# Kernel optimization log

Hardware: AMD Instinct MI355X
Metric: run time of the kernel (lower is better)

## Reference

```python
import jax, jax.numpy as jnp
import numpy as np

NUM_CLASSES = 10000
KREG = 5
LAMDA = 0.001
ALLOW_ZERO_SETS = False


def setup_inputs() -> dict:
    key = jax.random.key(0)
    k1, k2 = jax.random.split(key)
    logits = jax.random.normal(k1, (4096, NUM_CLASSES), dtype=jnp.float32)
    u = jax.random.uniform(k2, (4096,), dtype=jnp.float32)  # randomized tie-break draws
    T = jnp.asarray(1.3, dtype=jnp.float32)        # Platt temperature
    Qhat = jnp.asarray(0.9, dtype=jnp.float32)     # calibrated quantile threshold
    penalties = jnp.zeros((1, NUM_CLASSES), dtype=jnp.float32).at[:, KREG:].add(LAMDA)
    return {"logits": logits, "u": u, "T": T, "Qhat": Qhat, "penalties": penalties}


def reference(logits, u, T, Qhat, penalties):
    B, C = logits.shape
    scores = jax.nn.softmax(logits / T, axis=1)                  # [B, C]
    order = jnp.argsort(-scores, axis=1)                          # descending class indices
    ordered = jnp.take_along_axis(scores, order, axis=1)          # sorted scores, desc
    csum = jnp.cumsum(ordered, axis=1)                            # [B, C]
    pcs = jnp.cumsum(penalties, axis=1)                           # [1, C]
    # gcq: base set sizes via cumulative threshold
    sizes_base = jnp.sum((csum + pcs) <= Qhat, axis=1) + 1        # [B]
    sizes_base = jnp.minimum(sizes_base, C)
    # randomized rounding
    rows = jnp.arange(B)
    idx = jnp.maximum(sizes_base - 1, 0)
    ord_i = ordered[rows, idx]
    cs_i = csum[rows, idx]
    pc_i = pcs[0, idx]
    V = (Qhat - (cs_i - ord_i) - pc_i) / ord_i                    # [B]
    sizes = sizes_base - (u >= V).astype(sizes_base.dtype)
    sizes = jnp.where(Qhat == 1.0, C, sizes)
    if not ALLOW_ZERO_SETS:
        sizes = jnp.where(sizes == 0, 1, sizes)
    # Prediction sets S[i] = I[i, :sizes[i]] encoded as a dense membership mask.
    mask_sorted = jnp.arange(C)[None, :] < sizes[:, None]         # [B, C] in sorted order
    set_mask = jnp.zeros((B, C), dtype=jnp.int32).at[rows[:, None], order].set(
        mask_sorted.astype(jnp.int32)
    )
    return sizes.astype(jnp.int32), set_mask
```

## Files before the change

kernel.cpp:

```cpp
#include <hip/hip_runtime.h>

#define C_CLASSES 10000
#define THREADS 256
#define NWAVES (THREADS / 64)
#define ITEMS 40
#define FULL_CHUNKS 9
#define KCAP 1024
#define KMIN 905

struct SmemT {
  unsigned long long cand[KCAP];
  union {
    unsigned hist[2048];
    float scan[2][KCAP];
  } u;
  int sfx[THREADS];
  float redf[NWAVES];
  int redi[NWAVES];
  long long red64[NWAVES];
  unsigned long long bcast_cut;
  int cnt;
  int ssz_bcast;
};

__device__ __forceinline__ float block_max_f(float v, SmemT* sm) {
  #pragma unroll
  for (int m = 32; m; m >>= 1) v = fmaxf(v, __shfl_xor(v, m));
  if ((threadIdx.x & 63) == 0) sm->redf[threadIdx.x >> 6] = v;
  __syncthreads();
  float r = fmaxf(fmaxf(sm->redf[0], sm->redf[1]), fmaxf(sm->redf[2], sm->redf[3]));
  __syncthreads();
  return r;
}

__device__ __forceinline__ float block_sum_f(float v, SmemT* sm) {
  #pragma unroll
  for (int m = 32; m; m >>= 1) v += __shfl_xor(v, m);
  if ((threadIdx.x & 63) == 0) sm->redf[threadIdx.x >> 6] = v;
  __syncthreads();
  float r = (sm->redf[0] + sm->redf[1]) + (sm->redf[2] + sm->redf[3]);
  __syncthreads();
  return r;
}

__device__ __forceinline__ int block_min_i(int v, SmemT* sm) {
  #pragma unroll
  for (int m = 32; m; m >>= 1) { int o = __shfl_xor(v, m); v = (o < v) ? o : v; }
  if ((threadIdx.x & 63) == 0) sm->redi[threadIdx.x >> 6] = v;
  __syncthreads();
  int a = sm->redi[0] < sm->redi[1] ? sm->redi[0] : sm->redi[1];
  int b = sm->redi[2] < sm->redi[3] ? sm->redi[2] : sm->redi[3];
  int r = a < b ? a : b;
  __syncthreads();
  return r;
}

__device__ __forceinline__ long long block_max_ll(long long v, SmemT* sm) {
  #pragma unroll
  for (int m = 32; m; m >>= 1) { long long o = __shfl_xor(v, m); v = (o > v) ? o : v; }
  if ((threadIdx.x & 63) == 0) sm->red64[threadIdx.x >> 6] = v;
  __syncthreads();
  long long a = sm->red64[0] > sm->red64[1] ? sm->red64[0] : sm->red64[1];
  long long b = sm->red64[2] > sm->red64[3] ? sm->red64[2] : sm->red64[3];
  long long r = a > b ? a : b;
  __syncthreads();
  return r;
}

extern "C" __global__ void __launch_bounds__(THREADS)
conformal_kernel(const float* __restrict__ logits, const float* __restrict__ uvec,
                 const float* __restrict__ Tp, const float* __restrict__ Qp,
                 const float* __restrict__ pen, int* __restrict__ out_sizes,
                 int* __restrict__ out_mask)
{
  __shared__ SmemT sm;
  const int r = blockIdx.x;
  const int tid = threadIdx.x;
  const int lane = tid & 63;
  const float T = Tp[0];
  const float Qhat = Qp[0];
  const bool ones = (Qhat == 1.0f);
  const float* row = logits + (size_t)r * C_CLASSES;
  if (tid == 0) sm.cnt = 0;

  float sc[ITEMS];
  #pragma unroll
  for (int b = 0; b < FULL_CHUNKS; ++b) {
    float4 v = *reinterpret_cast<const float4*>(row + b * 1024 + tid * 4);
    sc[b*4+0] = v.x / T; sc[b*4+1] = v.y / T;
    sc[b*4+2] = v.z / T; sc[b*4+3] = v.w / T;
  }
  {
    int base = FULL_CHUNKS * 1024 + tid * 4;
    #pragma unroll
    for (int c2 = 0; c2 < 4; ++c2) {
      int j = base + c2;
      sc[36 + c2] = (j < C_CLASSES) ? (row[j] / T) : -INFINITY;
    }
  }
  float mx = -INFINITY;
  #pragma unroll
  for (int i = 0; i < ITEMS; ++i) mx = fmaxf(mx, sc[i]);
  mx = block_max_f(mx, &sm);

  float psum = 0.f;
  #pragma unroll
  for (int i = 0; i < ITEMS; ++i) { sc[i] = expf(sc[i] - mx); psum += sc[i]; }
  const float Z = block_sum_f(psum, &sm);
  #pragma unroll
  for (int i = 0; i < ITEMS; ++i) sc[i] = sc[i] / Z;

  unsigned thr = 0u;
  int base_above = 0;
  #pragma unroll
  for (int lvl = 0; lvl < 3; ++lvl) {
    const int sh = (lvl == 0) ? 21 : (lvl == 1) ? 10 : 0;
    const int width = (lvl < 2) ? 11 : 10;
    const int nb = 1 << width;
    const int g = nb / THREADS;
    const unsigned himask = (lvl == 0) ? 0u : ~((1u << (sh + width)) - 1u);
    for (int i = tid; i < nb; i += THREADS) sm.u.hist[i] = 0u;
    __syncthreads();
    #pragma unroll
    for (int i = 0; i < ITEMS; ++i) {
      unsigned kb = __float_as_uint(sc[i]);
      if ((kb & himask) == thr)
        atomicAdd(&sm.u.hist[(kb >> sh) & (nb - 1)], 1u);
    }
    __syncthreads();
    int loc[8]; int csum8 = 0;
    #pragma unroll
    for (int q = 7; q >= 0; --q)
      if (q < g) { csum8 += (int)sm.u.hist[tid * g + q]; loc[q] = csum8; }
    sm.sfx[tid] = csum8; __syncthreads();
    #pragma unroll
    for (int d = 1; d < THREADS; d <<= 1) {
      int v = sm.sfx[tid] + ((tid + d < THREADS) ? sm.sfx[tid + d] : 0);
      __syncthreads();
      sm.sfx[tid] = v;
      __syncthreads();
    }
    const int Sx = sm.sfx[tid] - csum8;
    long long best = -1ll;
    #pragma unroll
    for (int q = 0; q < 8; ++q) {
      if (q < g) {
        int n_incl = base_above + Sx + loc[q];
        if (n_incl >= KMIN) {
          long long p = ((long long)(tid * g + q) << 32) | (unsigned)n_incl;
          best = (p > best) ? p : best;
        }
      }
    }
    best = block_max_ll(best, &sm);
    const int b_sel = (int)(best >> 32);
    const int n_total = (int)(best & 0xFFFFFFFFll);
    thr |= ((unsigned)b_sel) << sh;
    if (n_total <= KCAP) break;
    base_above = n_total - (int)sm.u.hist[b_sel];
    __syncthreads();
  }

  #pragma unroll
  for (int i = 0; i < ITEMS; ++i) {
    unsigned kb = __float_as_uint(sc[i]);
    bool pred = (kb >= thr);
    unsigned long long mb = __ballot(pred);
    int base = 0;
    if (lane == 0) base = atomicAdd(&sm.cnt, (int)__popcll(mb));
    base = __shfl(base, 0);
    if (pred) {
      int off = __popcll(mb & ((1ull << lane) - 1ull));
      int pos = base + off;
      int j = (i >> 2) * 1024 + tid * 4 + (i & 3);
      if (pos < KCAP)
        sm.cand[pos] = (((unsigned long long)kb) << 16)
                     | (unsigned long long)(0xFFFF ^ j);
    }
  }
  __syncthreads();
  int cnt = sm.cnt; if (cnt > KCAP) cnt = KCAP;
  #pragma unroll
  for (int k = 0; k < KCAP / THREADS; ++k) {
    int p = tid + k * THREADS;
    if (p >= cnt) sm.cand[p] = 0ull;
  }
  __syncthreads();

  for (unsigned k = 2; k <= KCAP; k <<= 1) {
    for (unsigned stride = k >> 1; stride > 0; stride >>= 1) {
      #pragma unroll
      for (int rep = 0; rep < KCAP / THREADS; ++rep) {
        unsigned i = tid + rep * THREADS;
        unsigned partner = i ^ stride;
        if (partner > i) {
          unsigned long long a = sm.cand[i], b = sm.cand[partner];
          bool up = ((i & k) == 0);
          if (up ? (a < b) : (a > b)) { sm.cand[i] = b; sm.cand[partner] = a; }
        }
      }
      __syncthreads();
    }
  }

  #pragma unroll
  for (int k = 0; k < KCAP / THREADS; ++k) {
    int i = tid + k * THREADS;
    float val = __uint_as_float((unsigned)(sm.cand[i] >> 16));
    sm.u.scan[0][i] = val + pen[i];
  }
  __syncthreads();
  int src = 0;
  for (int d = 1; d < KCAP; d <<= 1) {
    #pragma unroll
    for (int k = 0; k < KCAP / THREADS; ++k) {
      int i = tid + k * THREADS;
      float v = sm.u.scan[src][i];
      if (i >= d) v += sm.u.scan[src][i - d];
      sm.u.scan[src ^ 1][i] = v;
    }
    src ^= 1;
    __syncthreads();
  }

  int floc = 0x7FFFFFFF;
  #pragma unroll
  for (int k = 0; k < KCAP / THREADS; ++k) {
    int i = tid + k * THREADS;
    if (sm.u.scan[src][i] > Qhat && i < floc) floc = i;
  }
  int f = block_min_i(floc, &sm);
  if (f > cnt - 1) f = cnt - 1;

  if (tid == 0) {
    float vf = __uint_as_float((unsigned)(sm.cand[f] >> 16));
    float comb = sm.u.scan[src][f];
    float V = ((Qhat - comb) + vf) / vf;
    int ssz = (f + 1) - ((uvec[r] >= V) ? 1 : 0);
    if (ones) ssz = C_CLASSES;
    if (ssz == 0) ssz = 1;
    out_sizes[r] = ssz;
    int cidx = ssz - 1;
    if (cidx > cnt - 1) cidx = cnt - 1;
    sm.bcast_cut = sm.cand[cidx];
    sm.ssz_bcast = ssz;
  }
  __syncthreads();
  const unsigned long long cut = sm.bcast_cut;

  int* mrow = out_mask + (size_t)r * C_CLASSES;
  #pragma unroll
  for (int b = 0; b < 10; ++b) {
    int j0 = b * 1024 + tid * 4;
    if (j0 < C_CLASSES) {
      int4 o;
      #pragma unroll
      for (int c2 = 0; c2 < 4; ++c2) {
        unsigned kb = __float_as_uint(sc[b * 4 + c2]);
        unsigned long long key = (((unsigned long long)kb) << 16)
                               | (unsigned long long)(0xFFFF ^ (j0 + c2));
        int m = (ones || key >= cut) ? 1 : 0;
        if (c2 == 0) o.x = m; else if (c2 == 1) o.y = m;
        else if (c2 == 2) o.z = m; else o.w = m;
      }
      *reinterpret_cast<int4*>(mrow + j0) = o;
    }
  }
}

extern "C" void kernel_launch(void* const* d_in, const int* in_sizes, int n_in,
                              void* d_out, int out_size, void* d_ws, size_t ws_size,
                              hipStream_t stream) {
  const float* logits = (const float*)d_in[0];
  const float* u      = (const float*)d_in[1];
  const float* Tp     = (const float*)d_in[2];
  const float* Qp     = (const float*)d_in[3];
  const float* pen    = (const float*)d_in[4];
  const int B = in_sizes[1];
  int* out_sizes = (int*)d_out;
  int* out_mask  = out_sizes + B;
  conformal_kernel<<<B, THREADS, 0, stream>>>(logits, u, Tp, Qp, pen, out_sizes, out_mask);
}
```

Baseline: 468.3 us.

## Replace LDS bitonic sort and scans with register/shuffle-based versions

Replaces the shared-memory bitonic sort of the 1024 candidates with a register-resident sort, four keys per thread. It uses intra-thread compares and wave shuffles, and only goes through LDS for the cross-wave strides. The Hillis-Steele histogram suffix scan and the cumulative-sum scan now use wave shuffles plus a small cross-wave combine. Penalties are staged into LDS, and launch bounds request 2 blocks per CU. This removes most of the per-stage barriers and LDS traffic, at the cost of more registers and shuffle instructions.

```diff
diff --git a/kernel.cpp b/kernel.cpp
--- a/kernel.cpp
+++ b/kernel.cpp
@@ -2,7 +2,6 @@
 
 #define C_CLASSES 10000
 #define THREADS 256
-#define NWAVES (THREADS / 64)
 #define ITEMS 40
 #define FULL_CHUNKS 9
 #define KCAP 1024
@@ -10,17 +9,14 @@
 
 struct SmemT {
   unsigned long long cand[KCAP];
-  union {
-    unsigned hist[2048];
-    float scan[2][KCAP];
-  } u;
-  int sfx[THREADS];
-  float redf[NWAVES];
-  int redi[NWAVES];
-  long long red64[NWAVES];
-  unsigned long long bcast_cut;
+  unsigned hist[2048];
+  float pen_s[KCAP];
+  float redf[4];
+  int redi[4];
+  long long red64[4];
+  float bc_vf, bc_comb;
+  unsigned long long bc_cut;
   int cnt;
-  int ssz_bcast;
 };
 
 __device__ __forceinline__ float block_max_f(float v, SmemT* sm) {
@@ -67,7 +63,41 @@
   return r;
 }
 
-extern "C" __global__ void __launch_bounds__(THREADS)
+__device__ __forceinline__ int wave_sfx_i(int v) {
+  int ln = threadIdx.x & 63;
+  #pragma unroll
+  for (int d = 1; d < 64; d <<= 1) {
+    int t = __shfl_down(v, d);
+    if (ln + d < 64) v += t;
+  }
+  return v;
+}
+
+__device__ __forceinline__ float wave_pfx_f(float v) {
+  int ln = threadIdx.x & 63;
+  #pragma unroll
+  for (int d = 1; d < 64; d <<= 1) {
+    float t = __shfl_up(v, d);
+    if (ln >= d) v += t;
+  }
+  return v;
+}
+
+__device__ __forceinline__ unsigned long long shfl_xor_u64(unsigned long long v, int m) {
+  unsigned lo = (unsigned)v, hi = (unsigned)(v >> 32);
+  lo = __shfl_xor(lo, m);
+  hi = __shfl_xor(hi, m);
+  return (((unsigned long long)hi) << 32) | lo;
+}
+
+__device__ __forceinline__ void cmpq(unsigned long long &a, unsigned long long &b, bool up) {
+  bool lt = (a < b);
+  unsigned long long mn = lt ? a : b, mx = lt ? b : a;
+  a = up ? mx : mn;
+  b = up ? mn : mx;
+}
+
+extern "C" __global__ void __launch_bounds__(THREADS, 2)
 conformal_kernel(const float* __restrict__ logits, const float* __restrict__ uvec,
                  const float* __restrict__ Tp, const float* __restrict__ Qp,
                  const float* __restrict__ pen, int* __restrict__ out_sizes,
@@ -77,10 +107,15 @@
   const int r = blockIdx.x;
   const int tid = threadIdx.x;
   const int lane = tid & 63;
+  const int w = tid >> 6;
   const float T = Tp[0];
   const float Qhat = Qp[0];
   const bool ones = (Qhat == 1.0f);
   const float* row = logits + (size_t)r * C_CLASSES;
+
+  #pragma unroll
+  for (int i = 0; i < KCAP / THREADS; ++i)
+    sm.pen_s[tid + i * THREADS] = pen[tid + i * THREADS];
   if (tid == 0) sm.cnt = 0;
 
   float sc[ITEMS];
@@ -112,43 +147,40 @@
 
   unsigned thr = 0u;
   int base_above = 0;
-  #pragma unroll
   for (int lvl = 0; lvl < 3; ++lvl) {
     const int sh = (lvl == 0) ? 21 : (lvl == 1) ? 10 : 0;
     const int width = (lvl < 2) ? 11 : 10;
     const int nb = 1 << width;
     const int g = nb / THREADS;
-    const unsigned himask = (lvl == 0) ? 0u : ~((1u << (sh + width)) - 1u);
-    for (int i = tid; i < nb; i += THREADS) sm.u.hist[i] = 0u;
+    const unsigned himask = (lvl == 0) ? 0u : (0xFFFFFFFFu << (sh + width));
+    for (int i = tid; i < nb; i += THREADS) sm.hist[i] = 0u;
     __syncthreads();
     #pragma unroll
     for (int i = 0; i < ITEMS; ++i) {
       unsigned kb = __float_as_uint(sc[i]);
       if ((kb & himask) == thr)
-        atomicAdd(&sm.u.hist[(kb >> sh) & (nb - 1)], 1u);
+        atomicAdd(&sm.hist[(kb >> sh) & (nb - 1)], 1u);
     }
     __syncthreads();
-    int loc[8]; int csum8 = 0;
+    int loc[8]; int ctot = 0;
     #pragma unroll
     for (int q = 7; q >= 0; --q)
-      if (q < g) { csum8 += (int)sm.u.hist[tid * g + q]; loc[q] = csum8; }
-    sm.sfx[tid] = csum8; __syncthreads();
-    #pragma unroll
-    for (int d = 1; d < THREADS; d <<= 1) {
-      int v = sm.sfx[tid] + ((tid + d < THREADS) ? sm.sfx[tid + d] : 0);
-      __syncthreads();
-      sm.sfx[tid] = v;
-      __syncthreads();
-    }
-    const int Sx = sm.sfx[tid] - csum8;
+      if (q < g) { ctot += (int)sm.hist[tid * g + q]; loc[q] = ctot; }
+    int incl = wave_sfx_i(ctot);
+    if (lane == 0) sm.redi[w] = incl;
+    __syncthreads();
+    int above = 0;
+    #pragma unroll
+    for (int w2 = 0; w2 < 4; ++w2) if (w2 > w) above += sm.redi[w2];
+    const int sfx = incl + above;
     long long best = -1ll;
     #pragma unroll
     for (int q = 0; q < 8; ++q) {
       if (q < g) {
-        int n_incl = base_above + Sx + loc[q];
+        int n_incl = base_above + (sfx - ctot) + loc[q];
         if (n_incl >= KMIN) {
           long long p = ((long long)(tid * g + q) << 32) | (unsigned)n_incl;
-          best = (p > best) ? p : best;
+          if (p > best) best = p;
         }
       }
     }
@@ -157,7 +189,7 @@
     const int n_total = (int)(best & 0xFFFFFFFFll);
     thr |= ((unsigned)b_sel) << sh;
     if (n_total <= KCAP) break;
-    base_above = n_total - (int)sm.u.hist[b_sel];
+    base_above = n_total - (int)sm.hist[b_sel];
     __syncthreads();
   }
 
@@ -187,54 +219,98 @@
   }
   __syncthreads();
 
-  for (unsigned k = 2; k <= KCAP; k <<= 1) {
-    for (unsigned stride = k >> 1; stride > 0; stride >>= 1) {
-      #pragma unroll
-      for (int rep = 0; rep < KCAP / THREADS; ++rep) {
-        unsigned i = tid + rep * THREADS;
-        unsigned partner = i ^ stride;
-        if (partner > i) {
-          unsigned long long a = sm.cand[i], b = sm.cand[partner];
-          bool up = ((i & k) == 0);
-          if (up ? (a < b) : (a > b)) { sm.cand[i] = b; sm.cand[partner] = a; }
-        }
-      }
-      __syncthreads();
-    }
-  }
-
-  #pragma unroll
-  for (int k = 0; k < KCAP / THREADS; ++k) {
-    int i = tid + k * THREADS;
-    float val = __uint_as_float((unsigned)(sm.cand[i] >> 16));
-    sm.u.scan[0][i] = val + pen[i];
-  }
-  __syncthreads();
-  int src = 0;
-  for (int d = 1; d < KCAP; d <<= 1) {
-    #pragma unroll
-    for (int k = 0; k < KCAP / THREADS; ++k) {
-      int i = tid + k * THREADS;
-      float v = sm.u.scan[src][i];
-      if (i >= d) v += sm.u.scan[src][i - d];
-      sm.u.scan[src ^ 1][i] = v;
-    }
-    src ^= 1;
-    __syncthreads();
-  }
+  unsigned long long k0 = sm.cand[tid*4+0];
+  unsigned long long k1 = sm.cand[tid*4+1];
+  unsigned long long k2 = sm.cand[tid*4+2];
+  unsigned long long k3 = sm.cand[tid*4+3];
+
+  #define XSTAGE(D, K4) { \
+    bool up_ = ((tid & (K4)) == 0); \
+    bool lo_ = ((tid & (D)) == 0); \
+    { unsigned long long P = shfl_xor_u64(k0, (D)); bool wm = (lo_ == up_); \
+      bool lt = (k0 < P); unsigned long long mn = lt ? k0 : P, mxv = lt ? P : k0; k0 = wm ? mxv : mn; } \
+    { unsigned long long P = shfl_xor_u64(k1, (D)); bool wm = (lo_ == up_); \
+      bool lt = (k1 < P); unsigned long long mn = lt ? k1 : P, mxv = lt ? P : k1; k1 = wm ? mxv : mn; } \
+    { unsigned long long P = shfl_xor_u64(k2, (D)); bool wm = (lo_ == up_); \
+      bool lt = (k2 < P); unsigned long long mn = lt ? k2 : P, mxv = lt ? P : k2; k2 = wm ? mxv : mn; } \
+    { unsigned long long P = shfl_xor_u64(k3, (D)); bool wm = (lo_ == up_); \
+      bool lt = (k3 < P); unsigned long long mn = lt ? k3 : P, mxv = lt ? P : k3; k3 = wm ? mxv : mn; } }
+
+  #define INTRA(K4) { \
+    bool up_ = ((tid & (K4)) == 0); \
+    cmpq(k0, k2, up_); cmpq(k1, k3, up_); \
+    cmpq(k0, k1, up_); cmpq(k2, k3, up_); }
+
+  #define LDSSTAGE(D, K4) { \
+    bool up_ = ((tid & (K4)) == 0); \
+    bool lo_ = ((tid & (D)) == 0); \
+    sm.cand[tid*4+0] = k0; sm.cand[tid*4+1] = k1; \
+    sm.cand[tid*4+2] = k2; sm.cand[tid*4+3] = k3; \
+    __syncthreads(); \
+    int pt_ = (tid ^ (D)) * 4; \
+    unsigned long long P0 = sm.cand[pt_+0], P1 = sm.cand[pt_+1]; \
+    unsigned long long P2 = sm.cand[pt_+2], P3 = sm.cand[pt_+3]; \
+    bool wm = (lo_ == up_); \
+    { bool lt = (k0 < P0); unsigned long long mn = lt ? k0 : P0, mxv = lt ? P0 : k0; k0 = wm ? mxv : mn; } \
+    { bool lt = (k1 < P1); unsigned long long mn = lt ? k1 : P1, mxv = lt ? P1 : k1; k1 = wm ? mxv : mn; } \
+    { bool lt = (k2 < P2); unsigned long long mn = lt ? k2 : P2, mxv = lt ? P2 : k2; k2 = wm ? mxv : mn; } \
+    { bool lt = (k3 < P3); unsigned long long mn = lt ? k3 : P3, mxv = lt ? P3 : k3; k3 = wm ? mxv : mn; } \
+    __syncthreads(); }
+
+  cmpq(k0, k1, true); cmpq(k2, k3, false);
+  { bool u_ = ((tid & 1) == 0); cmpq(k0, k2, u_); cmpq(k1, k3, u_); cmpq(k0, k1, u_); cmpq(k2, k3, u_); }
+  XSTAGE(1, 2)  INTRA(2)
+  XSTAGE(2, 4)  XSTAGE(1, 4)  INTRA(4)
+  XSTAGE(4, 8)  XSTAGE(2, 8)  XSTAGE(1, 8)  INTRA(8)
+  XSTAGE(8, 16) XSTAGE(4, 16) XSTAGE(2, 16) XSTAGE(1, 16) INTRA(16)
+  XSTAGE(16, 32) XSTAGE(8, 32) XSTAGE(4, 32) XSTAGE(2, 32) XSTAGE(1, 32) INTRA(32)
+  XSTAGE(32, 64) XSTAGE(16, 64) XSTAGE(8, 64) XSTAGE(4, 64) XSTAGE(2, 64) XSTAGE(1, 64) INTRA(64)
+  LDSSTAGE(64, 128)
+  XSTAGE(32, 128) XSTAGE(16, 128) XSTAGE(8, 128) XSTAGE(4, 128) XSTAGE(2, 128) XSTAGE(1, 128) INTRA(128)
+  LDSSTAGE(128, 256) LDSSTAGE(64, 256)
+  XSTAGE(32, 256) XSTAGE(16, 256) XSTAGE(8, 256) XSTAGE(4, 256) XSTAGE(2, 256) XSTAGE(1, 256) INTRA(256)
+
+  float v0 = __uint_as_float((unsigned)(k0 >> 16));
+  float v1 = __uint_as_float((unsigned)(k1 >> 16));
+  float v2 = __uint_as_float((unsigned)(k2 >> 16));
+  float v3 = __uint_as_float((unsigned)(k3 >> 16));
+  float p0 = sm.pen_s[tid*4+0], p1 = sm.pen_s[tid*4+1];
+  float p2 = sm.pen_s[tid*4+2], p3 = sm.pen_s[tid*4+3];
+  float c0 = v0 + p0;
+  float c1 = c0 + (v1 + p1);
+  float c2 = c1 + (v2 + p2);
+  float c3 = c2 + (v3 + p3);
+  float wincl = wave_pfx_f(c3);
+  float wbase = wincl - c3;
+  if (lane == 63) sm.redf[w] = wincl;
+  __syncthreads();
+  float cross = 0.f;
+  #pragma unroll
+  for (int w2 = 0; w2 < 4; ++w2) if (w2 < w) cross += sm.redf[w2];
+  const float basep = cross + wbase;
+  c0 += basep; c1 += basep; c2 += basep; c3 += basep;
 
   int floc = 0x7FFFFFFF;
-  #pragma unroll
-  for (int k = 0; k < KCAP / THREADS; ++k) {
-    int i = tid + k * THREADS;
-    if (sm.u.scan[src][i] > Qhat && i < floc) floc = i;
-  }
+  if      (c0 > Qhat) floc = tid*4+0;
+  else if (c1 > Qhat) floc = tid*4+1;
+  else if (c2 > Qhat) floc = tid*4+2;
+  else if (c3 > Qhat) floc = tid*4+3;
   int f = block_min_i(floc, &sm);
   if (f > cnt - 1) f = cnt - 1;
 
+  if ((f >> 2) == tid) {
+    int q = f & 3;
+    unsigned long long kk = (q==0)?k0:(q==1)?k1:(q==2)?k2:k3;
+    float cc = (q==0)?c0:(q==1)?c1:(q==2)?c2:c3;
+    sm.bc_vf = __uint_as_float((unsigned)(kk >> 16));
+    sm.bc_comb = cc;
+  }
+  sm.cand[tid*4+0] = k0; sm.cand[tid*4+1] = k1;
+  sm.cand[tid*4+2] = k2; sm.cand[tid*4+3] = k3;
+  __syncthreads();
+
   if (tid == 0) {
-    float vf = __uint_as_float((unsigned)(sm.cand[f] >> 16));
-    float comb = sm.u.scan[src][f];
+    float vf = sm.bc_vf, comb = sm.bc_comb;
     float V = ((Qhat - comb) + vf) / vf;
     int ssz = (f + 1) - ((uvec[r] >= V) ? 1 : 0);
     if (ones) ssz = C_CLASSES;
@@ -242,11 +318,10 @@
     out_sizes[r] = ssz;
     int cidx = ssz - 1;
     if (cidx > cnt - 1) cidx = cnt - 1;
-    sm.bcast_cut = sm.cand[cidx];
-    sm.ssz_bcast = ssz;
-  }
-  __syncthreads();
-  const unsigned long long cut = sm.bcast_cut;
+    sm.bc_cut = sm.cand[cidx];
+  }
+  __syncthreads();
+  const unsigned long long cut = sm.bc_cut;
 
   int* mrow = out_mask + (size_t)r * C_CLASSES;
   #pragma unroll
@@ -255,13 +330,13 @@
     if (j0 < C_CLASSES) {
       int4 o;
       #pragma unroll
-      for (int c2 = 0; c2 < 4; ++c2) {
-        unsigned kb = __float_as_uint(sc[b * 4 + c2]);
+      for (int c2i = 0; c2i < 4; ++c2i) {
+        unsigned kb = __float_as_uint(sc[b * 4 + c2i]);
         unsigned long long key = (((unsigned long long)kb) << 16)
-                               | (unsigned long long)(0xFFFF ^ (j0 + c2));
+                               | (unsigned long long)(0xFFFF ^ (j0 + c2i));
         int m = (ones || key >= cut) ? 1 : 0;
-        if (c2 == 0) o.x = m; else if (c2 == 1) o.y = m;
-        else if (c2 == 2) o.z = m; else o.w = m;
+        if (c2i == 0) o.x = m; else if (c2i == 1) o.y = m;
+        else if (c2i == 2) o.z = m; else o.w = m;
       }
       *reinterpret_cast<int4*>(mrow + j0) = o;
     }
```

Measured after the change: 380.2 us. 1.23x faster.

## Replace candidate sort and scan with sum-augmented radix select on threshold

Applied to the files above, without the earlier changes.

Drops the candidate compaction, the 1024-element bitonic sort and the shared-memory prefix scan. The three-level radix histogram now also accumulates per-bin probability sums, so the cumulative score at each bin boundary can be checked directly against Qhat plus the penalty prefix. A small search inside the final bin, plus tie resolution by index, gives the set size and the mask cut. Bin scans use wave shuffles instead of a shared-memory Hillis-Steele scan, and launch bounds request two blocks per CU. The cost is float atomics on shared memory, whose summation order differs from the sequential cumsum, and loops for ties that are rarely taken.

```diff
diff --git a/kernel.cpp b/kernel.cpp
--- a/kernel.cpp
+++ b/kernel.cpp
@@ -2,25 +2,21 @@
 
 #define C_CLASSES 10000
 #define THREADS 256
-#define NWAVES (THREADS / 64)
 #define ITEMS 40
 #define FULL_CHUNKS 9
-#define KCAP 1024
-#define KMIN 905
+#define RANK_CAP 905
 
 struct SmemT {
-  unsigned long long cand[KCAP];
-  union {
-    unsigned hist[2048];
-    float scan[2][KCAP];
-  } u;
-  int sfx[THREADS];
-  float redf[NWAVES];
-  int redi[NWAVES];
-  long long red64[NWAVES];
-  unsigned long long bcast_cut;
-  int cnt;
-  int ssz_bcast;
+  unsigned hcnt[2048];
+  float    hsum[2048];
+  float    pcs[1024];
+  float redf[4];
+  int   redi[4];
+  long long red64[4];
+  int   redc[4];
+  float redsf[4];
+  int   bc_Cab, bc_m, bc_ssz;
+  float bc_Sab;
 };
 
 __device__ __forceinline__ float block_max_f(float v, SmemT* sm) {
@@ -67,7 +63,26 @@
   return r;
 }
 
-extern "C" __global__ void __launch_bounds__(THREADS)
+__device__ __forceinline__ int wave_sfx_i(int v) {
+  int ln = threadIdx.x & 63;
+  #pragma unroll
+  for (int d = 1; d < 64; d <<= 1) { int t = __shfl_down(v, d); if (ln + d < 64) v += t; }
+  return v;
+}
+__device__ __forceinline__ float wave_sfx_f(float v) {
+  int ln = threadIdx.x & 63;
+  #pragma unroll
+  for (int d = 1; d < 64; d <<= 1) { float t = __shfl_down(v, d); if (ln + d < 64) v += t; }
+  return v;
+}
+__device__ __forceinline__ float wave_pfx_f(float v) {
+  int ln = threadIdx.x & 63;
+  #pragma unroll
+  for (int d = 1; d < 64; d <<= 1) { float t = __shfl_up(v, d); if (ln >= d) v += t; }
+  return v;
+}
+
+extern "C" __global__ void __launch_bounds__(THREADS, 2)
 conformal_kernel(const float* __restrict__ logits, const float* __restrict__ uvec,
                  const float* __restrict__ Tp, const float* __restrict__ Qp,
                  const float* __restrict__ pen, int* __restrict__ out_sizes,
@@ -77,11 +92,11 @@
   const int r = blockIdx.x;
   const int tid = threadIdx.x;
   const int lane = tid & 63;
+  const int w = tid >> 6;
   const float T = Tp[0];
   const float Qhat = Qp[0];
   const bool ones = (Qhat == 1.0f);
   const float* row = logits + (size_t)r * C_CLASSES;
-  if (tid == 0) sm.cnt = 0;
 
   float sc[ITEMS];
   #pragma unroll
@@ -98,6 +113,24 @@
       sc[36 + c2] = (j < C_CLASSES) ? (row[j] / T) : -INFINITY;
     }
   }
+
+  {
+    float p0 = pen[tid*4+0], p1 = pen[tid*4+1], p2 = pen[tid*4+2], p3 = pen[tid*4+3];
+    float s0 = p0, s1 = s0 + p1, s2 = s1 + p2, s3 = s2 + p3;
+    float wincl = wave_pfx_f(s3);
+    float wbase = wincl - s3;
+    if (lane == 63) sm.redsf[w] = wincl;
+    __syncthreads();
+    float cross = 0.f;
+    #pragma unroll
+    for (int w2 = 0; w2 < 4; ++w2) if (w2 < w) cross += sm.redsf[w2];
+    float basep = cross + wbase;
+    sm.pcs[tid*4+0] = basep + s0;
+    sm.pcs[tid*4+1] = basep + s1;
+    sm.pcs[tid*4+2] = basep + s2;
+    sm.pcs[tid*4+3] = basep + s3;
+  }
+
   float mx = -INFINITY;
   #pragma unroll
   for (int i = 0; i < ITEMS; ++i) mx = fmaxf(mx, sc[i]);
@@ -111,142 +144,131 @@
   for (int i = 0; i < ITEMS; ++i) sc[i] = sc[i] / Z;
 
   unsigned thr = 0u;
-  int base_above = 0;
-  #pragma unroll
+  int base_C = 0, m_dup = 0;
+  float base_S = 0.f;
   for (int lvl = 0; lvl < 3; ++lvl) {
     const int sh = (lvl == 0) ? 21 : (lvl == 1) ? 10 : 0;
     const int width = (lvl < 2) ? 11 : 10;
     const int nb = 1 << width;
     const int g = nb / THREADS;
-    const unsigned himask = (lvl == 0) ? 0u : ~((1u << (sh + width)) - 1u);
-    for (int i = tid; i < nb; i += THREADS) sm.u.hist[i] = 0u;
+    const unsigned himask = (lvl == 0) ? 0u : (0xFFFFFFFFu << (sh + width));
+    for (int i = tid; i < nb; i += THREADS) { sm.hcnt[i] = 0u; sm.hsum[i] = 0.f; }
     __syncthreads();
     #pragma unroll
     for (int i = 0; i < ITEMS; ++i) {
       unsigned kb = __float_as_uint(sc[i]);
-      if ((kb & himask) == thr)
-        atomicAdd(&sm.u.hist[(kb >> sh) & (nb - 1)], 1u);
-    }
-    __syncthreads();
-    int loc[8]; int csum8 = 0;
-    #pragma unroll
-    for (int q = 7; q >= 0; --q)
-      if (q < g) { csum8 += (int)sm.u.hist[tid * g + q]; loc[q] = csum8; }
-    sm.sfx[tid] = csum8; __syncthreads();
-    #pragma unroll
-    for (int d = 1; d < THREADS; d <<= 1) {
-      int v = sm.sfx[tid] + ((tid + d < THREADS) ? sm.sfx[tid + d] : 0);
-      __syncthreads();
-      sm.sfx[tid] = v;
-      __syncthreads();
-    }
-    const int Sx = sm.sfx[tid] - csum8;
+      if ((kb & himask) == thr) {
+        int b = (int)((kb >> sh) & (unsigned)(nb - 1));
+        atomicAdd(&sm.hcnt[b], 1u);
+        atomicAdd(&sm.hsum[b], sc[i]);
+      }
+    }
+    __syncthreads();
+    int locc[8]; float locs[8];
+    int ctot = 0; float stot = 0.f;
+    #pragma unroll
+    for (int q = 7; q >= 0; --q) if (q < g) {
+      ctot += (int)sm.hcnt[tid * g + q];
+      stot += sm.hsum[tid * g + q];
+      locc[q] = ctot; locs[q] = stot;
+    }
+    int sfx = wave_sfx_i(ctot);
+    float sfxf = wave_sfx_f(stot);
+    if (lane == 0) { sm.redc[w] = sfx; sm.redsf[w] = sfxf; }
+    __syncthreads();
+    int abv = 0; float abf = 0.f;
+    #pragma unroll
+    for (int w2 = 0; w2 < 4; ++w2) if (w2 > w) { abv += sm.redc[w2]; abf += sm.redsf[w2]; }
+    const int upc = base_C + abv + (sfx - ctot);
+    const float ups = base_S + abf + (sfxf - stot);
     long long best = -1ll;
     #pragma unroll
-    for (int q = 0; q < 8; ++q) {
-      if (q < g) {
-        int n_incl = base_above + Sx + loc[q];
-        if (n_incl >= KMIN) {
-          long long p = ((long long)(tid * g + q) << 32) | (unsigned)n_incl;
-          best = (p > best) ? p : best;
+    for (int q = 0; q < 8; ++q) if (q < g) {
+      int n_incl = upc + locc[q];
+      if (n_incl >= 1) {
+        int pidx = n_incl - 1; if (pidx > RANK_CAP - 1) pidx = RANK_CAP - 1;
+        float gl = ups + locs[q] + sm.pcs[pidx];
+        if (gl > Qhat) {
+          long long p = ((long long)(tid * g + q) << 32) | 1ll;
+          if (p > best) best = p;
         }
       }
     }
     best = block_max_ll(best, &sm);
-    const int b_sel = (int)(best >> 32);
-    const int n_total = (int)(best & 0xFFFFFFFFll);
+    const int b_sel = (best >= 0) ? (int)(best >> 32) : 0;
     thr |= ((unsigned)b_sel) << sh;
-    if (n_total <= KCAP) break;
-    base_above = n_total - (int)sm.u.hist[b_sel];
-    __syncthreads();
-  }
-
-  #pragma unroll
-  for (int i = 0; i < ITEMS; ++i) {
-    unsigned kb = __float_as_uint(sc[i]);
-    bool pred = (kb >= thr);
-    unsigned long long mb = __ballot(pred);
-    int base = 0;
-    if (lane == 0) base = atomicAdd(&sm.cnt, (int)__popcll(mb));
-    base = __shfl(base, 0);
-    if (pred) {
-      int off = __popcll(mb & ((1ull << lane) - 1ull));
-      int pos = base + off;
-      int j = (i >> 2) * 1024 + tid * 4 + (i & 3);
-      if (pos < KCAP)
-        sm.cand[pos] = (((unsigned long long)kb) << 16)
-                     | (unsigned long long)(0xFFFF ^ j);
-    }
-  }
-  __syncthreads();
-  int cnt = sm.cnt; if (cnt > KCAP) cnt = KCAP;
-  #pragma unroll
-  for (int k = 0; k < KCAP / THREADS; ++k) {
-    int p = tid + k * THREADS;
-    if (p >= cnt) sm.cand[p] = 0ull;
-  }
-  __syncthreads();
-
-  for (unsigned k = 2; k <= KCAP; k <<= 1) {
-    for (unsigned stride = k >> 1; stride > 0; stride >>= 1) {
-      #pragma unroll
-      for (int rep = 0; rep < KCAP / THREADS; ++rep) {
-        unsigned i = tid + rep * THREADS;
-        unsigned partner = i ^ stride;
-        if (partner > i) {
-          unsigned long long a = sm.cand[i], b = sm.cand[partner];
-          bool up = ((i & k) == 0);
-          if (up ? (a < b) : (a > b)) { sm.cand[i] = b; sm.cand[partner] = a; }
-        }
-      }
-      __syncthreads();
-    }
-  }
-
-  #pragma unroll
-  for (int k = 0; k < KCAP / THREADS; ++k) {
-    int i = tid + k * THREADS;
-    float val = __uint_as_float((unsigned)(sm.cand[i] >> 16));
-    sm.u.scan[0][i] = val + pen[i];
-  }
-  __syncthreads();
-  int src = 0;
-  for (int d = 1; d < KCAP; d <<= 1) {
-    #pragma unroll
-    for (int k = 0; k < KCAP / THREADS; ++k) {
-      int i = tid + k * THREADS;
-      float v = sm.u.scan[src][i];
-      if (i >= d) v += sm.u.scan[src][i - d];
-      sm.u.scan[src ^ 1][i] = v;
-    }
-    src ^= 1;
-    __syncthreads();
-  }
-
-  int floc = 0x7FFFFFFF;
-  #pragma unroll
-  for (int k = 0; k < KCAP / THREADS; ++k) {
-    int i = tid + k * THREADS;
-    if (sm.u.scan[src][i] > Qhat && i < floc) floc = i;
-  }
-  int f = block_min_i(floc, &sm);
-  if (f > cnt - 1) f = cnt - 1;
+    if (tid == b_sel / g) {
+      int q = b_sel - tid * g;
+      int n_incl = upc + locc[q];
+      float s_incl = ups + locs[q];
+      int nbin = (int)sm.hcnt[b_sel];
+      sm.bc_Cab = n_incl - nbin;
+      sm.bc_Sab = s_incl - sm.hsum[b_sel];
+      sm.bc_m = nbin;
+    }
+    __syncthreads();
+    base_C = sm.bc_Cab; base_S = sm.bc_Sab; m_dup = sm.bc_m;
+  }
+
+  const float vstar = __uint_as_float(thr);
+  const int C_above = base_C;
+  const float S_above = base_S;
+  int cap = RANK_CAP - C_above;
+  int ilim = (m_dup < cap) ? m_dup : cap;
+  if (ilim < 1) ilim = 1;
+  int iloc = 0x7FFFFFFF;
+  for (int ii = tid + 1; ii <= ilim; ii += THREADS) {
+    float gg = S_above + (float)ii * vstar + sm.pcs[C_above + ii - 1];
+    if (gg > Qhat) { iloc = ii; break; }
+  }
+  int isel = block_min_i(iloc, &sm);
+  if (isel == 0x7FFFFFFF) isel = ilim;
+  const int f = C_above + isel - 1;
 
   if (tid == 0) {
-    float vf = __uint_as_float((unsigned)(sm.cand[f] >> 16));
-    float comb = sm.u.scan[src][f];
-    float V = ((Qhat - comb) + vf) / vf;
+    float comb = S_above + (float)isel * vstar + sm.pcs[f];
+    float V = ((Qhat - comb) + vstar) / vstar;
     int ssz = (f + 1) - ((uvec[r] >= V) ? 1 : 0);
     if (ones) ssz = C_CLASSES;
     if (ssz == 0) ssz = 1;
     out_sizes[r] = ssz;
-    int cidx = ssz - 1;
-    if (cidx > cnt - 1) cidx = cnt - 1;
-    sm.bcast_cut = sm.cand[cidx];
-    sm.ssz_bcast = ssz;
-  }
-  __syncthreads();
-  const unsigned long long cut = sm.bcast_cut;
+    sm.bc_ssz = ssz;
+  }
+  __syncthreads();
+  const int ssz = sm.bc_ssz;
+
+  unsigned cutbits = thr;
+  int cutidx = 0x7FFFFFFF;
+  if (!ones) {
+    int kneed;
+    if (ssz - 1 == f) kneed = isel;
+    else if (isel >= 2) kneed = isel - 1;
+    else {
+      int mymin = 0x7FFFFFFF;
+      #pragma unroll
+      for (int i = 0; i < ITEMS; ++i) {
+        int kb = (int)__float_as_uint(sc[i]);
+        if (kb > (int)thr && kb < mymin) mymin = kb;
+      }
+      cutbits = (unsigned)block_min_i(mymin, &sm);
+      kneed = 0x7FFFFFFF;
+    }
+    if (kneed != 0x7FFFFFFF && kneed < m_dup) {
+      int excl = -1;
+      for (int t = 0; t < kneed; ++t) {
+        int cand = 0x7FFFFFFF;
+        #pragma unroll
+        for (int i = 0; i < ITEMS; ++i) {
+          if (__float_as_uint(sc[i]) == cutbits) {
+            int j = (i >> 2) * 1024 + tid * 4 + (i & 3);
+            if (j > excl && j < cand) cand = j;
+          }
+        }
+        excl = block_min_i(cand, &sm);
+      }
+      cutidx = excl;
+    }
+  }
 
   int* mrow = out_mask + (size_t)r * C_CLASSES;
   #pragma unroll
@@ -257,11 +279,10 @@
       #pragma unroll
       for (int c2 = 0; c2 < 4; ++c2) {
         unsigned kb = __float_as_uint(sc[b * 4 + c2]);
-        unsigned long long key = (((unsigned long long)kb) << 16)
-                               | (unsigned long long)(0xFFFF ^ (j0 + c2));
-        int m = (ones || key >= cut) ? 1 : 0;
-        if (c2 == 0) o.x = m; else if (c2 == 1) o.y = m;
-        else if (c2 == 2) o.z = m; else o.w = m;
+        int j = j0 + c2;
+        int mbit = (ones || kb > cutbits || (kb == cutbits && j <= cutidx)) ? 1 : 0;
+        if (c2 == 0) o.x = mbit; else if (c2 == 1) o.y = mbit;
+        else if (c2 == 2) o.z = mbit; else o.w = mbit;
       }
       *reinterpret_cast<int4*>(mrow + j0) = o;
     }
```

Result: slower. 531.7 us (+13.5%).
